# Optimization experiments

Hardware: AMD Instinct MI355X
Metric: run time of the kernel (lower is better)

Reference implementation:

```python
import jax, jax.numpy as jnp
import numpy as np

# Config from init_kwargs
B = 16
CIN = 128
COUT = 256
N = 16        # num_filters
L = 32        # length
K = 3         # kernel_size
KAPPA = 4
STRIDE = 1
PAD = 2
LP = L + PAD  # padded spatial length for FFT


def make_wn():
    # DFT-derived channel-mixing matrix, (cin, d) with d = cout // n
    v = np.arange(CIN)[:, None]
    sr = N * CIN // COUT
    inds = np.arange(CIN)[np.arange(CIN) % sr == 0]
    M = v @ v[inds].T  # (cin, d)
    wn = np.exp((2j * np.pi / CIN) * M) / CIN
    return jnp.asarray(wn.astype(np.complex64))


def setup_inputs() -> dict:
    key = jax.random.key(0)
    k1, k2 = jax.random.split(key)
    x = jax.random.normal(k1, (B, CIN, L, L), dtype=jnp.float32)
    rng = float(np.sqrt(KAPPA / (CIN * K * K)))
    weight = (jax.random.uniform(k2, (N, CIN // KAPPA, K, K), dtype=jnp.float32) - 0.5) * 2.0 * rng
    return {"x": x, "weight": weight}


def reference(x, weight):
    wn = make_wn()  # complex64 (CIN, COUT//N), constant buffer
    # 3D real FFT over (channel, h, w); weight zero-padded from cin//kappa -> cin channels
    x_hat = jnp.fft.rfftn(x, s=(CIN, LP, LP), axes=(-3, -2, -1))          # (B, CIN, LP, LP//2+1)
    w_hat = jnp.fft.rfftn(weight, s=(CIN, LP, LP), axes=(-3, -2, -1))     # (N, CIN, LP, LP//2+1)
    freq = jnp.einsum('bchw,nchw->bnchw', x_hat, w_hat)                   # broadcast, no reduction
    out = jnp.fft.irfftn(freq, s=(LP, LP), axes=(-2, -1))                 # real (B, N, CIN, LP, LP)
    # complex channel mix contracting c -> d; result complex, take real part
    out = jnp.einsum('cd,bnchw->bndhw', wn, out)                          # (B, N, D, LP, LP) complex
    out = out.real[:, :, :, PAD:, PAD:]                                   # (B, N, D, L, L)
    out = jnp.transpose(out, (0, 2, 1, 3, 4))                             # (B, D, N, L, L)
    out = out.reshape(out.shape[0], -1, out.shape[3], out.shape[4])       # (B, COUT, L, L)
    if STRIDE == 2:
        idx = jnp.arange(0, L, 2)
        out = out[:, :, idx, :][:, :, :, idx]
    return out
```

## Files before the change

### kernel.cpp

```cpp
#include <hip/hip_runtime.h>
#include <hip/hip_bf16.h>


typedef __attribute__((ext_vector_type(8))) short short8;
typedef __attribute__((ext_vector_type(4))) float floatx4;

#define NT 256
#define LCH 168
#define SROWS 34
#define XSROW (SROWS * LCH)

__global__ __launch_bounds__(NT, 2)
void fconv_mfma(const float* __restrict__ x,
                const float* __restrict__ wgt,
                float* __restrict__ out) {
    __shared__ __align__(16) short xs[4 * XSROW];

    const int rq  = blockIdx.x;
    const int b   = blockIdx.y;
    const int r0  = rq * 2;
    const int tid = threadIdx.x;
    const int lane = tid & 63;
    const int wv  = tid >> 6;

    const int n = lane & 15;
    const int q = lane >> 4;

    float wreg[72];
    {
        const float4* wp = (const float4*)(wgt + (n * 288 + q * 72));
#pragma unroll
        for (int i = 0; i < 18; ++i) {
            const float4 t4 = wp[i];
            wreg[4 * i]     = t4.x; wreg[4 * i + 1] = t4.y;
            wreg[4 * i + 2] = t4.z; wreg[4 * i + 3] = t4.w;
        }
    }
    short8 af[9];
#pragma unroll
    for (int t = 0; t < 9; ++t)
#pragma unroll
        for (int j = 0; j < 8; ++j) {
            const int f = (7 - j) * 9 + (8 - t);
            __hip_bfloat16 hh = __float2bfloat16(0.5f * wreg[f]);
            af[t][j] = __builtin_bit_cast(short, hh);
        }

    const int ch = tid & 127;
    const int h  = tid >> 7;
    const bool w1 = (ch <= 64);
    const bool w2 = (ch >= 33);
#pragma unroll
    for (int rr = 0; rr < 2; ++rr) {
        const int lrow = 2 * h + rr;
        const int grow = r0 + lrow;
        short* rowbase = &xs[lrow * XSROW];
        if (grow < 32) {
            const float* rowp = x + ((size_t)((b * 128 + ch) * 32 + grow) << 5);
#pragma unroll
            for (int cq = 0; cq < 8; ++cq) {
                const float4 v4 = *(const float4*)(rowp + cq * 4);
                const float vv[4] = {v4.x, v4.y, v4.z, v4.w};
#pragma unroll
                for (int e = 0; e < 4; ++e) {
                    const int col = cq * 4 + e;
                    __hip_bfloat16 hb = __float2bfloat16(vv[e]);
                    const short hv = __builtin_bit_cast(short, hb);
                    if (w1) rowbase[col * LCH + ch + 95] = hv;
                    if (w2) rowbase[col * LCH + ch - 33] = hv;
                }
            }
        } else {
#pragma unroll
            for (int col = 0; col < 32; ++col) {
                if (w1) rowbase[col * LCH + ch + 95] = 0;
                if (w2) rowbase[col * LCH + ch - 33] = 0;
            }
        }
    }
    if (tid < 168) {
        const int row = tid / 42;
        const int g   = tid - row * 42;
        short8 z = {0, 0, 0, 0, 0, 0, 0, 0};
        *(short8*)&xs[(row * SROWS + 32) * LCH + g * 8] = z;
    }

    __syncthreads();

    const int lr = wv >> 1;
    const int sh = wv & 1;
    const int s0 = sh << 4;
    const int bpi = (lr * SROWS + s0 + n) * LCH - 8 * q;

    for (int d = 0; d <= 8; ++d) {
        floatx4 a0 = {0.f, 0.f, 0.f, 0.f}, a1 = {0.f, 0.f, 0.f, 0.f};
        floatx4 b0 = {0.f, 0.f, 0.f, 0.f}, b1 = {0.f, 0.f, 0.f, 0.f};
#pragma unroll
        for (int u = 0; u < 3; ++u)
#pragma unroll
            for (int v = 0; v < 3; ++v) {
                const int t = u * 3 + v;
                const int si = bpi + (u * SROWS + v) * LCH;
                const short8 ba = *(const short8*)&xs[si + 8 * (11 + d)];
                const short8 bb = *(const short8*)&xs[si + 8 * (11 - d)];
                if (t & 1) {
                    a1 = __builtin_amdgcn_mfma_f32_16x16x32_bf16(af[t], ba, a1, 0, 0, 0);
                    b1 = __builtin_amdgcn_mfma_f32_16x16x32_bf16(af[t], bb, b1, 0, 0, 0);
                } else {
                    a0 = __builtin_amdgcn_mfma_f32_16x16x32_bf16(af[t], ba, a0, 0, 0, 0);
                    b0 = __builtin_amdgcn_mfma_f32_16x16x32_bf16(af[t], bb, b0, 0, 0, 0);
                }
            }
        const floatx4 acc = (a0 + a1) + (b0 + b1);
        float* op = out + ((size_t)((b * 256 + d * 16 + q * 4) * 32 + (r0 + lr)) << 5) + s0 + n;
        op[0]    = acc.x;
        op[1024] = acc.y;
        op[2048] = acc.z;
        op[3072] = acc.w;
        if (d >= 1 && d <= 7) {
            float* op2 = op + (size_t)(16 - 2 * d) * 16384;
            op2[0]    = acc.x;
            op2[1024] = acc.y;
            op2[2048] = acc.z;
            op2[3072] = acc.w;
        }
    }
}

extern "C" void kernel_launch(void* const* d_in, const int* in_sizes, int n_in,
                              void* d_out, int out_size, void* d_ws, size_t ws_size,
                              hipStream_t stream) {
    const float* x   = (const float*)d_in[0];
    const float* wgt = (const float*)d_in[1];
    float* out = (float*)d_out;
    (void)in_sizes; (void)n_in; (void)out_size; (void)d_ws; (void)ws_size;

    fconv_mfma<<<dim3(16, 16), dim3(NT), 0, stream>>>(x, wgt, out);
}
```

Baseline: 74.54 us.

## Split frequency loop across twice the waves and restage inputs via LDS

Doubles the block to 512 threads and splits the nine output frequency indices between two wave groups, each handling its share with a fully unrolled templated routine. For d=0 and d=8 the mirrored product is replaced by doubling the single accumulator, which drops redundant MFMAs. Weights are converted to bf16 once into shared memory instead of each thread loading 72 floats. The input is restaged with a single 16-byte vectorized LDS write per element group instead of scalar duplicate writes. In exchange the block needs more threads and extra LDS, and the global input loads become strided gathers across channels.

```diff
diff --git a/kernel.cpp b/kernel.cpp
--- a/kernel.cpp
+++ b/kernel.cpp
@@ -5,125 +5,141 @@
 typedef __attribute__((ext_vector_type(8))) short short8;
 typedef __attribute__((ext_vector_type(4))) float floatx4;
 
-#define NT 256
+#define NT 512
 #define LCH 168
 #define SROWS 34
 #define XSROW (SROWS * LCH)
+
+template<int D, bool DUP>
+__device__ __forceinline__ void compute_d(const char* basep, const short8 af[9],
+                                          float* opbase) {
+    floatx4 a0 = {0.f,0.f,0.f,0.f}, a1 = {0.f,0.f,0.f,0.f};
+    floatx4 b0 = {0.f,0.f,0.f,0.f}, b1 = {0.f,0.f,0.f,0.f};
+#pragma unroll
+    for (int u = 0; u < 3; ++u)
+#pragma unroll
+        for (int v = 0; v < 3; ++v) {
+            const int t = u * 3 + v;
+            const short8 ba = *(const short8*)(basep +
+                ((u * SROWS + v) * LCH + 8 * (8 + D)) * 2);
+            if (t & 1) a1 = __builtin_amdgcn_mfma_f32_16x16x32_bf16(af[t], ba, a1, 0, 0, 0);
+            else       a0 = __builtin_amdgcn_mfma_f32_16x16x32_bf16(af[t], ba, a0, 0, 0, 0);
+            if (!DUP) {
+                const short8 bb = *(const short8*)(basep +
+                    ((u * SROWS + v) * LCH + 8 * (8 - D)) * 2);
+                if (t & 1) b1 = __builtin_amdgcn_mfma_f32_16x16x32_bf16(af[t], bb, b1, 0, 0, 0);
+                else       b0 = __builtin_amdgcn_mfma_f32_16x16x32_bf16(af[t], bb, b0, 0, 0, 0);
+            }
+        }
+    floatx4 acc = a0 + a1;
+    if (DUP) acc = acc + acc;
+    else     acc = acc + (b0 + b1);
+    float* op = opbase + D * 16384;
+    op[0]    = acc.x;
+    op[1024] = acc.y;
+    op[2048] = acc.z;
+    op[3072] = acc.w;
+    if (D >= 1 && D <= 7) {
+        float* op2 = opbase + (16 - D) * 16384;
+        op2[0]    = acc.x;
+        op2[1024] = acc.y;
+        op2[2048] = acc.z;
+        op2[3072] = acc.w;
+    }
+}
 
 __global__ __launch_bounds__(NT, 2)
 void fconv_mfma(const float* __restrict__ x,
                 const float* __restrict__ wgt,
                 float* __restrict__ out) {
     __shared__ __align__(16) short xs[4 * XSROW];
+    __shared__ __align__(16) short wf[9 * 640];
 
-    const int rq  = blockIdx.x;
-    const int b   = blockIdx.y;
-    const int r0  = rq * 2;
-    const int tid = threadIdx.x;
+    const int rq   = blockIdx.x;
+    const int b    = blockIdx.y;
+    const int r0   = rq * 2;
+    const int tid  = threadIdx.x;
     const int lane = tid & 63;
-    const int wv  = tid >> 6;
+    const int wv   = tid >> 6;
 
-    const int n = lane & 15;
-    const int q = lane >> 4;
-
-    float wreg[72];
     {
-        const float4* wp = (const float4*)(wgt + (n * 288 + q * 72));
+        const int n  = tid >> 5;
+        const int c2 = tid & 31;
+        const float* wb = wgt + (size_t)(n * 32 + c2) * 9;
+        const int pos = n * 40 + (c2 & 24) + (7 - (c2 & 7));
 #pragma unroll
-        for (int i = 0; i < 18; ++i) {
-            const float4 t4 = wp[i];
-            wreg[4 * i]     = t4.x; wreg[4 * i + 1] = t4.y;
-            wreg[4 * i + 2] = t4.z; wreg[4 * i + 3] = t4.w;
+        for (int k = 0; k < 9; ++k) {
+            __hip_bfloat16 h = __float2bfloat16(0.5f * wb[k]);
+            wf[(8 - k) * 640 + pos] = __builtin_bit_cast(short, h);
         }
     }
-    short8 af[9];
+
+    const float* xb_base = x + ((size_t)b << 17);
 #pragma unroll
-    for (int t = 0; t < 9; ++t)
+    for (int it = 0; it < 5; ++it) {
+        const int idx  = wv * 320 + it * 64 + lane;
+        const int col  = idx & 31;
+        const int rest = idx >> 5;
+        const int lrow = rest & 3;
+        const int oL   = rest >> 2;
+        const int grow = r0 + lrow;
+        short8 g;
+        if (grow < 32) {
+            float v[8];
 #pragma unroll
-        for (int j = 0; j < 8; ++j) {
-            const int f = (7 - j) * 9 + (8 - t);
-            __hip_bfloat16 hh = __float2bfloat16(0.5f * wreg[f]);
-            af[t][j] = __builtin_bit_cast(short, hh);
+            for (int j = 0; j < 8; ++j) {
+                const int m = (oL * 8 + j - 95) & 127;
+                v[j] = xb_base[((m << 5) + grow) * 32 + col];
+            }
+            union { __hip_bfloat162 h2[4]; short8 s8; } u;
+#pragma unroll
+            for (int p = 0; p < 4; ++p)
+                u.h2[p] = __float22bfloat162_rn(make_float2(v[2 * p], v[2 * p + 1]));
+            g = u.s8;
+        } else {
+            g = short8{0, 0, 0, 0, 0, 0, 0, 0};
         }
-
-    const int ch = tid & 127;
-    const int h  = tid >> 7;
-    const bool w1 = (ch <= 64);
-    const bool w2 = (ch >= 33);
-#pragma unroll
-    for (int rr = 0; rr < 2; ++rr) {
-        const int lrow = 2 * h + rr;
-        const int grow = r0 + lrow;
-        short* rowbase = &xs[lrow * XSROW];
-        if (grow < 32) {
-            const float* rowp = x + ((size_t)((b * 128 + ch) * 32 + grow) << 5);
-#pragma unroll
-            for (int cq = 0; cq < 8; ++cq) {
-                const float4 v4 = *(const float4*)(rowp + cq * 4);
-                const float vv[4] = {v4.x, v4.y, v4.z, v4.w};
-#pragma unroll
-                for (int e = 0; e < 4; ++e) {
-                    const int col = cq * 4 + e;
-                    __hip_bfloat16 hb = __float2bfloat16(vv[e]);
-                    const short hv = __builtin_bit_cast(short, hb);
-                    if (w1) rowbase[col * LCH + ch + 95] = hv;
-                    if (w2) rowbase[col * LCH + ch - 33] = hv;
-                }
-            }
-        } else {
-#pragma unroll
-            for (int col = 0; col < 32; ++col) {
-                if (w1) rowbase[col * LCH + ch + 95] = 0;
-                if (w2) rowbase[col * LCH + ch - 33] = 0;
-            }
-        }
+        *(short8*)&xs[(lrow * SROWS + col) * LCH + oL * 8] = g;
     }
-    if (tid < 168) {
-        const int row = tid / 42;
-        const int g   = tid - row * 42;
+    if (tid < 160) {
+        const int oL   = tid % 20;
+        const int rem  = tid / 20;
+        const int lrow = rem >> 1;
+        const int col  = 32 + (rem & 1);
         short8 z = {0, 0, 0, 0, 0, 0, 0, 0};
-        *(short8*)&xs[(row * SROWS + 32) * LCH + g * 8] = z;
+        *(short8*)&xs[(lrow * SROWS + col) * LCH + oL * 8] = z;
     }
 
     __syncthreads();
 
-    const int lr = wv >> 1;
-    const int sh = wv & 1;
-    const int s0 = sh << 4;
-    const int bpi = (lr * SROWS + s0 + n) * LCH - 8 * q;
+    const int n = lane & 15;
+    const int q = lane >> 4;
+    short8 af[9];
+#pragma unroll
+    for (int t = 0; t < 9; ++t)
+        af[t] = *(const short8*)&wf[t * 640 + n * 40 + q * 8];
 
-    for (int d = 0; d <= 8; ++d) {
-        floatx4 a0 = {0.f, 0.f, 0.f, 0.f}, a1 = {0.f, 0.f, 0.f, 0.f};
-        floatx4 b0 = {0.f, 0.f, 0.f, 0.f}, b1 = {0.f, 0.f, 0.f, 0.f};
-#pragma unroll
-        for (int u = 0; u < 3; ++u)
-#pragma unroll
-            for (int v = 0; v < 3; ++v) {
-                const int t = u * 3 + v;
-                const int si = bpi + (u * SROWS + v) * LCH;
-                const short8 ba = *(const short8*)&xs[si + 8 * (11 + d)];
-                const short8 bb = *(const short8*)&xs[si + 8 * (11 - d)];
-                if (t & 1) {
-                    a1 = __builtin_amdgcn_mfma_f32_16x16x32_bf16(af[t], ba, a1, 0, 0, 0);
-                    b1 = __builtin_amdgcn_mfma_f32_16x16x32_bf16(af[t], bb, b1, 0, 0, 0);
-                } else {
-                    a0 = __builtin_amdgcn_mfma_f32_16x16x32_bf16(af[t], ba, a0, 0, 0, 0);
-                    b0 = __builtin_amdgcn_mfma_f32_16x16x32_bf16(af[t], bb, b0, 0, 0, 0);
-                }
-            }
-        const floatx4 acc = (a0 + a1) + (b0 + b1);
-        float* op = out + ((size_t)((b * 256 + d * 16 + q * 4) * 32 + (r0 + lr)) << 5) + s0 + n;
-        op[0]    = acc.x;
-        op[1024] = acc.y;
-        op[2048] = acc.z;
-        op[3072] = acc.w;
-        if (d >= 1 && d <= 7) {
-            float* op2 = op + (size_t)(16 - 2 * d) * 16384;
-            op2[0]    = acc.x;
-            op2[1024] = acc.y;
-            op2[2048] = acc.z;
-            op2[3072] = acc.w;
-        }
+    const int tile = wv & 3;
+    const int lr   = tile >> 1;
+    const int sh   = tile & 1;
+    const int s0   = sh << 4;
+    const int dg   = wv >> 2;
+
+    const char* basep = (const char*)xs +
+        ((lr * SROWS + s0 + n) * LCH + 8 * (3 - q)) * 2;
+    float* opbase = out + ((size_t)((b * 256 + q * 4) * 32 + (r0 + lr)) << 5) + s0 + n;
+
+    if (dg == 0) {
+        compute_d<0, true >(basep, af, opbase);
+        compute_d<2, false>(basep, af, opbase);
+        compute_d<4, false>(basep, af, opbase);
+        compute_d<6, false>(basep, af, opbase);
+        compute_d<8, true >(basep, af, opbase);
+    } else {
+        compute_d<1, false>(basep, af, opbase);
+        compute_d<3, false>(basep, af, opbase);
+        compute_d<5, false>(basep, af, opbase);
+        compute_d<7, false>(basep, af, opbase);
     }
 }
 
```

Measured after the change: 70.47 us. 5.5% less time.
